# Performance work log

Hardware: AMD Instinct MI355X
Metric: run time of the kernel (lower is better)

The kernel has to match this reference:

```python
import jax, jax.numpy as jnp
import numpy as np

N_KW = 65536
N_DOC = 65536
N = N_KW + N_DOC
D_NODE = 128   # kw_size == middle_dim
D_MID = 128
D_FB = 16
D_T = 8
E = 1048576


def setup_inputs() -> dict:
    key = jax.random.key(0)
    ks = jax.random.split(key, 14)
    X_nodes = jax.random.normal(ks[0], (N, D_NODE), jnp.float32)
    X_feedback = jax.random.normal(ks[1], (N_DOC, D_FB), jnp.float32)
    X_time = jax.random.normal(ks[2], (N_DOC, D_T), jnp.float32)
    src = jax.random.randint(ks[3], (E,), 0, N_KW)            # kw node ids
    dst = N_KW + jax.random.randint(ks[4], (E,), 0, N_DOC)    # doc node ids
    edge_kw2doc = jnp.stack([src, dst])                       # [2, E], row0=src
    edge_doc2kw = jnp.stack([dst, src])

    def lin(k, fan_in, fan_out):
        return jax.random.normal(k, (fan_in, fan_out), jnp.float32) / np.sqrt(fan_in).astype(np.float32)

    params = dict(
        W0=lin(ks[5], D_NODE, D_MID), b0=jnp.zeros((D_MID,), jnp.float32),
        Wg1=lin(ks[6], D_MID, D_MID), bg1=jnp.zeros((D_MID,), jnp.float32),
        Wg2=lin(ks[7], D_MID, D_MID), bg2=jnp.zeros((D_MID,), jnp.float32),
        Wf1=lin(ks[8], D_FB, D_MID), bf1=jnp.zeros((D_MID,), jnp.float32),
        Wf2=lin(ks[9], D_MID, D_MID), bf2=jnp.zeros((D_MID,), jnp.float32),
        Wt1=lin(ks[10], D_T, D_MID), bt1=jnp.zeros((D_MID,), jnp.float32),
        Wt2=lin(ks[11], D_MID, D_MID), bt2=jnp.zeros((D_MID,), jnp.float32),
    )
    return {"X_nodes": X_nodes, "X_feedback": X_feedback, "X_time": X_time,
            "edge_kw2doc": edge_kw2doc, "edge_doc2kw": edge_doc2kw, "n_kw": N_KW, **params}


def _gcn(x, edge, W, b, n):
    # PyG GCNConv: add self-loops, symmetric normalization deg^{-1/2} A deg^{-1/2}, then linear.
    loop = jnp.arange(n)
    srcs = jnp.concatenate([edge[0], loop])
    dsts = jnp.concatenate([edge[1], loop])
    deg = jax.ops.segment_sum(jnp.ones(srcs.shape[0], x.dtype), dsts, num_segments=n)
    dis = jnp.where(deg > 0, jax.lax.rsqrt(jnp.maximum(deg, 1e-12)), jnp.zeros((), x.dtype))
    norm = dis[srcs] * dis[dsts]
    h = x @ W                                   # [N, D_MID]
    msg = h[srcs] * norm[:, None]               # gather on src, [E+N, D_MID]
    return jax.ops.segment_sum(msg, dsts, num_segments=n) + b


def reference(X_nodes, X_feedback, X_time, edge_kw2doc, edge_doc2kw, n_kw,
              W0, b0, Wg1, bg1, Wg2, bg2, Wf1, bf1, Wf2, bf2, Wt1, bt1, Wt2, bt2):
    n = X_nodes.shape[0]
    # feedback / time MLPs (relu on all but last layer)
    xf = jax.nn.relu(X_feedback @ Wf1 + bf1) @ Wf2 + bf2   # [N_DOC, D_MID]
    xt = jax.nn.relu(X_time @ Wt1 + bt1) @ Wt2 + bt2       # [N_DOC, D_MID]
    # layer 0: Linear on kw nodes only; doc rows stay zero
    x = jnp.zeros((n, W0.shape[1]), X_nodes.dtype)
    x = x.at[:n_kw].set(jax.nn.relu(X_nodes[:n_kw] @ W0 + b0))
    # layer 1: GCNConv kw2doc, write doc rows
    x2 = jax.nn.relu(_gcn(x, edge_kw2doc, Wg1, bg1, n))
    x = x.at[n_kw:].set(x2[n_kw:])
    # layer 2: GCNConv doc2kw, write kw rows
    x2 = jax.nn.relu(_gcn(x, edge_doc2kw, Wg2, bg2, n))
    x = x.at[:n_kw].set(x2[:n_kw])
    # merge_f (Mul) then merge_t (Mul) on doc rows
    x = x.at[n_kw:].mul(xf)
    x = x.at[n_kw:].mul(xt)
    return x
```

## Files before the change

### kernel.cpp

```cpp
#include <hip/hip_runtime.h>

#define NKW   65536
#define NDOC  65536
#define NSEG  131072
#define NE    1048576
#define CHUNK 4096
#define NBLK  (NE / CHUNK)

typedef unsigned long long u64;
typedef unsigned short     u16;
typedef unsigned int       u32;
typedef unsigned char      u8;

typedef __attribute__((ext_vector_type(8))) short short8;
typedef __attribute__((ext_vector_type(4))) float f32x4;
typedef __attribute__((ext_vector_type(2))) float f32x2;

union U8 { short8 v; u64 u[2]; short s[8]; };

__device__ __forceinline__ u16 f2bf(float f) {
    u32 u = __builtin_bit_cast(u32, f);
    u = (u + 0x7fffu + ((u >> 16) & 1u)) >> 16;
    return (u16)u;
}
__device__ __forceinline__ float bf2f(u16 h) {
    return __builtin_bit_cast(float, (u32)h << 16);
}
__device__ __forceinline__ u8 f2fp8(float f) {
    u32 pk = __builtin_amdgcn_cvt_pk_fp8_f32(f, f, 0u, false);
    return (u8)pk;
}

#define BUFA_OFF 0ull
#define BUFD_OFF 8388608ull
#define BUFB_OFF 16777216ull
#define BUFC_OFF 33554432ull
#define WF_OFF   50331648ull
#define CSR_OFF  51380224ull
#define CNT_OFF  59768832ull
#define AUX_OFF  60293120ull
#define OFF_OFF  60821504ull
#define DIS_OFF  61345792ull

#define WOFF_W0  0
#define WOFF_WG1 2048
#define WOFF_WG2 4096
#define WOFF_WF1 6144
#define WOFF_WF2 8192
#define WOFF_WT1 10240
#define WOFF_WT2 12288

struct PrepArgs { const float* w[7]; int K[7]; };

__global__ void zero_k(int* __restrict__ p) {
    p[blockIdx.x * 256 + threadIdx.x] = 0;
}

__global__ __launch_bounds__(256) void k1_hist_prep(
        const int* __restrict__ src, const int* __restrict__ dst,
        int* __restrict__ bhist, PrepArgs pa, short8* __restrict__ wfb) {
    __shared__ int h[512];
    const int tid = threadIdx.x;
    if (blockIdx.x < NBLK) {
        for (int i = tid; i < 512; i += 256) h[i] = 0;
        __syncthreads();
        int e0 = blockIdx.x * CHUNK;
        for (int i = tid; i < CHUNK; i += 256) {
            int s = src[e0 + i];
            int d = dst[e0 + i] - NKW;
            atomicAdd(&h[s >> 8], 1);
            atomicAdd(&h[256 + (d >> 8)], 1);
        }
        __syncthreads();
        for (int i = tid; i < 512; i += 256)
            if (h[i]) atomicAdd(&bhist[i], h[i]);
    } else {
        int u = (blockIdx.x - NBLK) * 4 + (tid >> 6);
        if (u < 224) {
            int m = u >> 5, bk = u & 31;
            int kc = bk >> 3, ct = bk & 7;
            int l = tid & 63;
            int K = pa.K[m];
            const float* W = pa.w[m];
            U8 o;
            #pragma unroll
            for (int i = 0; i < 8; ++i) {
                int k   = kc * 32 + 4 * (l >> 4) + (i & 3) + 16 * (i >> 2);
                int col = ct * 16 + (l & 15);
                float v = (k < K) ? W[(size_t)k * 128 + col] : 0.f;
                o.s[i] = (short)f2bf(v);
            }
            wfb[(size_t)m * 2048 + bk * 64 + l] = o.v;
        }
    }
}

__global__ __launch_bounds__(256) void k2_part(
        const int* __restrict__ src, const int* __restrict__ dst,
        const int* __restrict__ bhist, int* __restrict__ bfill,
        u32* __restrict__ pairs) {
    __shared__ int h[512], sc[512], base[512], gb[512];
    __shared__ u32 staged[2 * CHUNK];
    const int tid = threadIdx.x;

    for (int i = tid; i < 512; i += 256) gb[i] = bhist[i];
    __syncthreads();
    for (int d = 1; d < 512; d <<= 1) {
        int i1 = tid + 256;
        int t0 = (tid >= d) ? gb[tid - d] : 0;
        int t1 = gb[i1 - d];
        __syncthreads();
        gb[tid] += t0; gb[i1] += t1;
        __syncthreads();
    }
    for (int i = tid; i < 512; i += 256) gb[i] -= bhist[i];
    for (int i = tid; i < 512; i += 256) h[i] = 0;
    __syncthreads();

    const int e0 = blockIdx.x * CHUNK;
    int se[16], de[16];
    #pragma unroll
    for (int j = 0; j < 16; ++j) {
        int e = e0 + tid + j * 256;
        se[j] = src[e];
        de[j] = dst[e] - NKW;
        atomicAdd(&h[se[j] >> 8], 1);
        atomicAdd(&h[256 + (de[j] >> 8)], 1);
    }
    __syncthreads();

    sc[tid] = h[tid];
    __syncthreads();
    for (int d = 1; d < 256; d <<= 1) {
        int t = (tid >= d) ? sc[tid - d] : 0;
        __syncthreads();
        sc[tid] += t;
        __syncthreads();
    }
    sc[256 + tid] = h[256 + tid];
    __syncthreads();
    for (int d = 1; d < 256; d <<= 1) {
        int t = (tid >= d) ? sc[256 + tid - d] : 0;
        __syncthreads();
        sc[256 + tid] += t;
        __syncthreads();
    }

    for (int i = tid; i < 512; i += 256) {
        base[i] = gb[i] + atomicAdd(&bfill[i], h[i]);
        sc[i] -= h[i];
        h[i] = 0;
    }
    __syncthreads();

    #pragma unroll
    for (int j = 0; j < 16; ++j) {
        int bk = se[j] >> 8;
        int r  = atomicAdd(&h[bk], 1);
        staged[sc[bk] + r] = ((u32)(se[j] & 255) << 16) | (u32)de[j];
        int bd = 256 + (de[j] >> 8);
        int r2 = atomicAdd(&h[bd], 1);
        staged[CHUNK + sc[bd] + r2] = ((u32)(de[j] & 255) << 16) | (u32)se[j];
    }
    __syncthreads();

    for (int i = tid; i < 512; i += 256) {
        int n = h[i];
        int so = (i < 256 ? 0 : CHUNK) + sc[i];
        u32* dp = pairs + base[i];
        for (int j = 0; j < n; ++j) dp[j] = staged[so + j];
    }
}

__global__ __launch_bounds__(256) void k3_build(
        const u32* __restrict__ pairs, const int* __restrict__ bhist,
        int* __restrict__ off, int* __restrict__ cnt,
        float* __restrict__ dis, int* __restrict__ csr) {
    __shared__ int lcnt[256], loff[256], bs[256], gsc[512];
    const int tid = threadIdx.x;
    const int b = blockIdx.x;
    for (int i = tid; i < 512; i += 256) gsc[i] = bhist[i];
    __syncthreads();
    for (int d = 1; d < 512; d <<= 1) {
        int i1 = tid + 256;
        int t0 = (tid >= d) ? gsc[tid - d] : 0;
        int t1 = gsc[i1 - d];
        __syncthreads();
        gsc[tid] += t0; gsc[i1] += t1;
        __syncthreads();
    }
    const int size  = bhist[b];
    const int start = gsc[b] - size;
    lcnt[tid] = 0;
    __syncthreads();
    for (int i = tid; i < size; i += 256)
        atomicAdd(&lcnt[(pairs[start + i] >> 16) & 255], 1);
    __syncthreads();
    int s = lcnt[tid];
    bs[tid] = s;
    __syncthreads();
    for (int d = 1; d < 256; d <<= 1) {
        int t = (tid >= d) ? bs[tid - d] : 0;
        __syncthreads();
        bs[tid] += t;
        __syncthreads();
    }
    const int P = bs[tid] - s;
    const int seg = (b < 256) ? (b * 256 + tid) : (NKW + (b - 256) * 256 + tid);
    off[seg] = start + P;
    cnt[seg] = s;
    dis[seg] = rsqrtf((float)(s + 1));
    loff[tid] = P;
    lcnt[tid] = 0;
    __syncthreads();
    for (int i = tid; i < size; i += 256) {
        u32 p = pairs[start + i];
        int key = (p >> 16) & 255;
        int r = atomicAdd(&lcnt[key], 1);
        csr[start + loff[key] + r] = (int)(p & 0xFFFF);
    }
}

__global__ __launch_bounds__(256) void k45_gemm0_gates(
        const float* __restrict__ Xn, const short8* __restrict__ wfb,
        const float* __restrict__ b0, u8* __restrict__ h0f8,
        const float* __restrict__ Xfb, const float* __restrict__ Xt,
        const float* __restrict__ bf1v, const float* __restrict__ bf2v,
        const float* __restrict__ bt1v, const float* __restrict__ bt2v,
        u16* __restrict__ g) {
    __shared__ u16 H[64][136];
    const int tid = threadIdx.x;
    const int w = tid >> 6, l = tid & 63, lr = l & 15, q = l >> 4;

    if (blockIdx.x >= 1024) {
        const int blk = blockIdx.x - 1024;
        const int row = blk * 64 + w * 16 + lr;
        f32x4 acc[8];
        #pragma unroll
        for (int ct = 0; ct < 8; ++ct) acc[ct] = (f32x4){0.f, 0.f, 0.f, 0.f};
        #pragma unroll
        for (int kc = 0; kc < 4; ++kc) {
            U8 a;
            const int kb = kc * 32 + 4 * q;
            const float* A = Xn + (size_t)row * 128;
            f32x4 lo = *(const f32x4*)(A + kb);
            f32x4 hi = *(const f32x4*)(A + kb + 16);
            #pragma unroll
            for (int i = 0; i < 4; ++i) {
                a.s[i]     = (short)f2bf(lo[i]);
                a.s[4 + i] = (short)f2bf(hi[i]);
            }
            #pragma unroll
            for (int ct = 0; ct < 8; ++ct)
                acc[ct] = __builtin_amdgcn_mfma_f32_16x16x32_bf16(
                              a.v, wfb[WOFF_W0 + (kc * 8 + ct) * 64 + l], acc[ct], 0, 0, 0);
        }
        const int orow0 = blk * 64 + w * 16 + 4 * q;
        #pragma unroll
        for (int ct = 0; ct < 8; ++ct) {
            const int col = ct * 16 + lr;
            const float bb = b0[col];
            #pragma unroll
            for (int r = 0; r < 4; ++r) {
                float v = fmaxf(acc[ct][r] + bb, 0.f);
                h0f8[(size_t)(orow0 + r) * 128 + col] = f2fp8(v);
            }
        }
        return;
    }

    const int blk  = blockIdx.x;
    const int row0 = blk * 64 + w * 16;
    const int lrow = w * 16 + lr;
    const int orow = w * 16 + 4 * q;

    f32x4 acc[8];
    {
        U8 a;
        f32x4 x = *(const f32x4*)(Xfb + (size_t)(row0 + lr) * 16 + 4 * q);
        #pragma unroll
        for (int i = 0; i < 4; ++i) { a.s[i] = (short)f2bf(x[i]); a.s[4 + i] = 0; }
        #pragma unroll
        for (int ct = 0; ct < 8; ++ct)
            acc[ct] = __builtin_amdgcn_mfma_f32_16x16x32_bf16(
                          a.v, wfb[WOFF_WF1 + ct * 64 + l], (f32x4){0.f,0.f,0.f,0.f}, 0, 0, 0);
    }
    #pragma unroll
    for (int ct = 0; ct < 8; ++ct) {
        const int col = ct * 16 + lr;
        const float bb = bf1v[col];
        #pragma unroll
        for (int r = 0; r < 4; ++r)
            H[orow + r][col] = f2bf(fmaxf(acc[ct][r] + bb, 0.f));
    }
    __threadfence_block();

    f32x4 accf[8];
    #pragma unroll
    for (int ct = 0; ct < 8; ++ct) accf[ct] = (f32x4){0.f, 0.f, 0.f, 0.f};
    #pragma unroll
    for (int kc = 0; kc < 4; ++kc) {
        U8 a;
        const int kb = kc * 32 + 4 * q;
        a.u[0] = *(const u64*)&H[lrow][kb];
        a.u[1] = *(const u64*)&H[lrow][kb + 16];
        #pragma unroll
        for (int ct = 0; ct < 8; ++ct)
            accf[ct] = __builtin_amdgcn_mfma_f32_16x16x32_bf16(
                           a.v, wfb[WOFF_WF2 + (kc * 8 + ct) * 64 + l], accf[ct], 0, 0, 0);
    }
    __threadfence_block();

    {
        U8 a;
        #pragma unroll
        for (int i = 0; i < 8; ++i) a.s[i] = 0;
        if (q < 2) {
            f32x4 x = *(const f32x4*)(Xt + (size_t)(row0 + lr) * 8 + 4 * q);
            #pragma unroll
            for (int i = 0; i < 4; ++i) a.s[i] = (short)f2bf(x[i]);
        }
        #pragma unroll
        for (int ct = 0; ct < 8; ++ct)
            acc[ct] = __builtin_amdgcn_mfma_f32_16x16x32_bf16(
                          a.v, wfb[WOFF_WT1 + ct * 64 + l], (f32x4){0.f,0.f,0.f,0.f}, 0, 0, 0);
    }
    #pragma unroll
    for (int ct = 0; ct < 8; ++ct) {
        const int col = ct * 16 + lr;
        const float bb = bt1v[col];
        #pragma unroll
        for (int r = 0; r < 4; ++r)
            H[orow + r][col] = f2bf(fmaxf(acc[ct][r] + bb, 0.f));
    }
    __threadfence_block();

    f32x4 acct[8];
    #pragma unroll
    for (int ct = 0; ct < 8; ++ct) acct[ct] = (f32x4){0.f, 0.f, 0.f, 0.f};
    #pragma unroll
    for (int kc = 0; kc < 4; ++kc) {
        U8 a;
        const int kb = kc * 32 + 4 * q;
        a.u[0] = *(const u64*)&H[lrow][kb];
        a.u[1] = *(const u64*)&H[lrow][kb + 16];
        #pragma unroll
        for (int ct = 0; ct < 8; ++ct)
            acct[ct] = __builtin_amdgcn_mfma_f32_16x16x32_bf16(
                           a.v, wfb[WOFF_WT2 + (kc * 8 + ct) * 64 + l], acct[ct], 0, 0, 0);
    }
    #pragma unroll
    for (int ct = 0; ct < 8; ++ct) {
        const int col = ct * 16 + lr;
        const float b2f = bf2v[col];
        const float b2t = bt2v[col];
        #pragma unroll
        for (int r = 0; r < 4; ++r) {
            float gv = (accf[ct][r] + b2f) * (acct[ct][r] + b2t);
            g[(size_t)(blk * 64 + orow + r) * 128 + col] = f2bf(gv);
        }
    }
}

template<bool KW_SIDE>
__global__ __launch_bounds__(256) void aggf8_k(
        const int* __restrict__ off, const int* __restrict__ cnt,
        const int* __restrict__ csr, const u8* __restrict__ gsrc,
        const u8* __restrict__ h0f8, const float* __restrict__ dis,
        u16* __restrict__ outb) {
    const int r    = blockIdx.x * 16 + (threadIdx.x >> 4);
    const int lane = threadIdx.x & 15;
    const int seg  = KW_SIDE ? r : (NKW + r);
    const int st = off[seg];
    const int n  = cnt[seg];
    float a[8];
    #pragma unroll
    for (int j = 0; j < 8; ++j) a[j] = 0.f;

    #define DECACC(vv) { \
        u32 lo_ = (u32)(vv), hi_ = (u32)((vv) >> 32); \
        f32x2 p0 = __builtin_amdgcn_cvt_pk_f32_fp8(lo_, false); \
        f32x2 p1 = __builtin_amdgcn_cvt_pk_f32_fp8(lo_, true);  \
        f32x2 p2 = __builtin_amdgcn_cvt_pk_f32_fp8(hi_, false); \
        f32x2 p3 = __builtin_amdgcn_cvt_pk_f32_fp8(hi_, true);  \
        a[0] += p0[0]; a[1] += p0[1]; a[2] += p1[0]; a[3] += p1[1]; \
        a[4] += p2[0]; a[5] += p2[1]; a[6] += p3[0]; a[7] += p3[1]; }

    int i = 0;
    for (; i + 8 <= n; i += 8) {
        int nb[8];
        #pragma unroll
        for (int k = 0; k < 8; ++k) nb[k] = csr[st + i + k];
        u64 v[8];
        #pragma unroll
        for (int k = 0; k < 8; ++k)
            v[k] = *(const u64*)(gsrc + (size_t)nb[k] * 128 + lane * 8);
        #pragma unroll
        for (int k = 0; k < 8; ++k) DECACC(v[k])
    }
    for (; i < n; ++i) {
        int nb = csr[st + i];
        u64 v = *(const u64*)(gsrc + (size_t)nb * 128 + lane * 8);
        DECACC(v)
    }
    #undef DECACC

    const float dk = dis[seg];
    if (KW_SIDE) {
        u64 hv = *(const u64*)(h0f8 + (size_t)r * 128 + lane * 8);
        u32 lo_ = (u32)hv, hi_ = (u32)(hv >> 32);
        f32x2 p0 = __builtin_amdgcn_cvt_pk_f32_fp8(lo_, false);
        f32x2 p1 = __builtin_amdgcn_cvt_pk_f32_fp8(lo_, true);
        f32x2 p2 = __builtin_amdgcn_cvt_pk_f32_fp8(hi_, false);
        f32x2 p3 = __builtin_amdgcn_cvt_pk_f32_fp8(hi_, true);
        float hh[8] = {p0[0], p0[1], p1[0], p1[1], p2[0], p2[1], p3[0], p3[1]};
        #pragma unroll
        for (int j = 0; j < 8; ++j) a[j] = dk * (a[j] + dk * hh[j]);
    } else {
        #pragma unroll
        for (int j = 0; j < 8; ++j) a[j] *= dk;
    }
    U8 o;
    #pragma unroll
    for (int j = 0; j < 8; ++j) o.s[j] = (short)f2bf(a[j]);
    *(short8*)(outb + (size_t)r * 128 + lane * 8) = o.v;
}

__global__ __launch_bounds__(256) void k7_gemm1g(
        const u16* __restrict__ aggin, const short8* __restrict__ wfb,
        const float* __restrict__ bg1, const u16* __restrict__ gmul,
        u8* __restrict__ xdocf8, float* __restrict__ outdoc) {
    const int tid = threadIdx.x;
    const int w = tid >> 6, l = tid & 63, lr = l & 15, q = l >> 4;
    const int row = blockIdx.x * 64 + w * 16 + lr;
    f32x4 acc[8];
    #pragma unroll
    for (int ct = 0; ct < 8; ++ct) acc[ct] = (f32x4){0.f, 0.f, 0.f, 0.f};
    #pragma unroll
    for (int kc = 0; kc < 4; ++kc) {
        U8 a;
        const int kb = kc * 32 + 4 * q;
        const u16* A = aggin + (size_t)row * 128;
        a.u[0] = *(const u64*)(A + kb);
        a.u[1] = *(const u64*)(A + kb + 16);
        #pragma unroll
        for (int ct = 0; ct < 8; ++ct)
            acc[ct] = __builtin_amdgcn_mfma_f32_16x16x32_bf16(
                          a.v, wfb[WOFF_WG1 + (kc * 8 + ct) * 64 + l], acc[ct], 0, 0, 0);
    }
    const int orow0 = blockIdx.x * 64 + w * 16 + 4 * q;
    #pragma unroll
    for (int ct = 0; ct < 8; ++ct) {
        const int col = ct * 16 + lr;
        const float bb = bg1[col];
        #pragma unroll
        for (int r = 0; r < 4; ++r) {
            float v = fmaxf(acc[ct][r] + bb, 0.f);
            const size_t idx = (size_t)(orow0 + r) * 128 + col;
            xdocf8[idx] = f2fp8(v);
            float o = v * bf2f(gmul[idx]);
            __builtin_nontemporal_store(o, outdoc + idx);
        }
    }
}

__global__ __launch_bounds__(256) void k8_gemm2(
        const u16* __restrict__ Av, const short8* __restrict__ wfb,
        const float* __restrict__ bg2, float* __restrict__ outf32) {
    const int tid = threadIdx.x;
    const int w = tid >> 6, l = tid & 63, lr = l & 15, q = l >> 4;
    const int row = blockIdx.x * 64 + w * 16 + lr;
    f32x4 acc[8];
    #pragma unroll
    for (int ct = 0; ct < 8; ++ct) acc[ct] = (f32x4){0.f, 0.f, 0.f, 0.f};
    #pragma unroll
    for (int kc = 0; kc < 4; ++kc) {
        U8 a;
        const int kb = kc * 32 + 4 * q;
        const u16* A = Av + (size_t)row * 128;
        a.u[0] = *(const u64*)(A + kb);
        a.u[1] = *(const u64*)(A + kb + 16);
        #pragma unroll
        for (int ct = 0; ct < 8; ++ct)
            acc[ct] = __builtin_amdgcn_mfma_f32_16x16x32_bf16(
                          a.v, wfb[WOFF_WG2 + (kc * 8 + ct) * 64 + l], acc[ct], 0, 0, 0);
    }
    const int orow0 = blockIdx.x * 64 + w * 16 + 4 * q;
    #pragma unroll
    for (int ct = 0; ct < 8; ++ct) {
        const int col = ct * 16 + lr;
        const float bb = bg2[col];
        #pragma unroll
        for (int r = 0; r < 4; ++r) {
            float v = fmaxf(acc[ct][r] + bb, 0.f);
            __builtin_nontemporal_store(v, outf32 + (size_t)(orow0 + r) * 128 + col);
        }
    }
}

extern "C" void kernel_launch(void* const* d_in, const int* in_sizes, int n_in,
                              void* d_out, int out_size, void* d_ws, size_t ws_size,
                              hipStream_t stream) {
    const float* Xn  = (const float*)d_in[0];
    const float* Xfb = (const float*)d_in[1];
    const float* Xt  = (const float*)d_in[2];
    const int*   e01 = (const int*)d_in[3];
    const float* W0  = (const float*)d_in[6];
    const float* b0  = (const float*)d_in[7];
    const float* Wg1 = (const float*)d_in[8];
    const float* bg1 = (const float*)d_in[9];
    const float* Wg2 = (const float*)d_in[10];
    const float* bg2 = (const float*)d_in[11];
    const float* Wf1 = (const float*)d_in[12];
    const float* bf1 = (const float*)d_in[13];
    const float* Wf2 = (const float*)d_in[14];
    const float* bf2 = (const float*)d_in[15];
    const float* Wt1 = (const float*)d_in[16];
    const float* bt1 = (const float*)d_in[17];
    const float* Wt2 = (const float*)d_in[18];
    const float* bt2 = (const float*)d_in[19];

    float* out = (float*)d_out;
    char*  ws  = (char*)d_ws;
    u8*    bufA  = (u8*)(ws + BUFA_OFF);
    u8*    bufD  = (u8*)(ws + BUFD_OFF);
    u16*   bufB  = (u16*)(ws + BUFB_OFF);
    u16*   bufC  = (u16*)(ws + BUFC_OFF);
    u32*   pairs = (u32*)(ws + BUFC_OFF);
    short8* wfb  = (short8*)(ws + WF_OFF);
    int*   csr   = (int*)(ws + CSR_OFF);
    int*   cnt   = (int*)(ws + CNT_OFF);
    int*   bhist = (int*)(ws + AUX_OFF);
    int*   bfill = bhist + 512;
    int*   off   = (int*)(ws + OFF_OFF);
    float* dis   = (float*)(ws + DIS_OFF);

    const int* src = e01;
    const int* dst = e01 + NE;

    PrepArgs pa;
    pa.w[0] = W0;  pa.K[0] = 128;
    pa.w[1] = Wg1; pa.K[1] = 128;
    pa.w[2] = Wg2; pa.K[2] = 128;
    pa.w[3] = Wf1; pa.K[3] = 16;
    pa.w[4] = Wf2; pa.K[4] = 128;
    pa.w[5] = Wt1; pa.K[5] = 8;
    pa.w[6] = Wt2; pa.K[6] = 128;

    zero_k<<<4, 256, 0, stream>>>(bhist);
    k1_hist_prep<<<NBLK + 56, 256, 0, stream>>>(src, dst, bhist, pa, wfb);
    k2_part<<<NBLK, 256, 0, stream>>>(src, dst, bhist, bfill, pairs);
    k3_build<<<512, 256, 0, stream>>>(pairs, bhist, off, cnt, dis, csr);
    k45_gemm0_gates<<<2048, 256, 0, stream>>>(Xn, wfb, b0, bufA,
                                              Xfb, Xt, bf1, bf2, bt1, bt2, bufB);

    aggf8_k<false><<<NDOC / 16, 256, 0, stream>>>(off, cnt, csr, bufA, nullptr, dis, bufC);
    k7_gemm1g<<<1024, 256, 0, stream>>>(bufC, wfb, bg1, bufB, bufD,
                                        out + (size_t)NKW * 128);

    aggf8_k<true><<<NKW / 16, 256, 0, stream>>>(off, cnt, csr, bufD, bufA, dis, bufC);
    k8_gemm2<<<1024, 256, 0, stream>>>(bufC, wfb, bg2, out);
}
```

Before: 166.1 us.

## Fuse gate MLP into partition kernel and gemm0 into CSR build kernel

Merges the independent feedback/time gate MLP blocks into the edge-partition launch and the layer-0 GEMM blocks into the CSR build launch, removing one kernel launch. Independent work now runs alongside the latency-bound graph preprocessing kernels and can fill idle CUs. The gate blocks reuse the partition kernel's shared staging buffer for their H tile. The partition kernel's larger shared footprint now applies to the gate blocks too, which may lower their occupancy.

```diff
diff --git a/kernel.cpp b/kernel.cpp
--- a/kernel.cpp
+++ b/kernel.cpp
@@ -95,181 +95,93 @@
     }
 }
 
-__global__ __launch_bounds__(256) void k2_part(
+__global__ __launch_bounds__(256) void k2_part_gates(
         const int* __restrict__ src, const int* __restrict__ dst,
         const int* __restrict__ bhist, int* __restrict__ bfill,
-        u32* __restrict__ pairs) {
-    __shared__ int h[512], sc[512], base[512], gb[512];
-    __shared__ u32 staged[2 * CHUNK];
-    const int tid = threadIdx.x;
-
-    for (int i = tid; i < 512; i += 256) gb[i] = bhist[i];
-    __syncthreads();
-    for (int d = 1; d < 512; d <<= 1) {
-        int i1 = tid + 256;
-        int t0 = (tid >= d) ? gb[tid - d] : 0;
-        int t1 = gb[i1 - d];
-        __syncthreads();
-        gb[tid] += t0; gb[i1] += t1;
-        __syncthreads();
-    }
-    for (int i = tid; i < 512; i += 256) gb[i] -= bhist[i];
-    for (int i = tid; i < 512; i += 256) h[i] = 0;
-    __syncthreads();
-
-    const int e0 = blockIdx.x * CHUNK;
-    int se[16], de[16];
-    #pragma unroll
-    for (int j = 0; j < 16; ++j) {
-        int e = e0 + tid + j * 256;
-        se[j] = src[e];
-        de[j] = dst[e] - NKW;
-        atomicAdd(&h[se[j] >> 8], 1);
-        atomicAdd(&h[256 + (de[j] >> 8)], 1);
-    }
-    __syncthreads();
-
-    sc[tid] = h[tid];
-    __syncthreads();
-    for (int d = 1; d < 256; d <<= 1) {
-        int t = (tid >= d) ? sc[tid - d] : 0;
-        __syncthreads();
-        sc[tid] += t;
-        __syncthreads();
-    }
-    sc[256 + tid] = h[256 + tid];
-    __syncthreads();
-    for (int d = 1; d < 256; d <<= 1) {
-        int t = (tid >= d) ? sc[256 + tid - d] : 0;
-        __syncthreads();
-        sc[256 + tid] += t;
-        __syncthreads();
-    }
-
-    for (int i = tid; i < 512; i += 256) {
-        base[i] = gb[i] + atomicAdd(&bfill[i], h[i]);
-        sc[i] -= h[i];
-        h[i] = 0;
-    }
-    __syncthreads();
-
-    #pragma unroll
-    for (int j = 0; j < 16; ++j) {
-        int bk = se[j] >> 8;
-        int r  = atomicAdd(&h[bk], 1);
-        staged[sc[bk] + r] = ((u32)(se[j] & 255) << 16) | (u32)de[j];
-        int bd = 256 + (de[j] >> 8);
-        int r2 = atomicAdd(&h[bd], 1);
-        staged[CHUNK + sc[bd] + r2] = ((u32)(de[j] & 255) << 16) | (u32)se[j];
-    }
-    __syncthreads();
-
-    for (int i = tid; i < 512; i += 256) {
-        int n = h[i];
-        int so = (i < 256 ? 0 : CHUNK) + sc[i];
-        u32* dp = pairs + base[i];
-        for (int j = 0; j < n; ++j) dp[j] = staged[so + j];
-    }
-}
-
-__global__ __launch_bounds__(256) void k3_build(
-        const u32* __restrict__ pairs, const int* __restrict__ bhist,
-        int* __restrict__ off, int* __restrict__ cnt,
-        float* __restrict__ dis, int* __restrict__ csr) {
-    __shared__ int lcnt[256], loff[256], bs[256], gsc[512];
-    const int tid = threadIdx.x;
-    const int b = blockIdx.x;
-    for (int i = tid; i < 512; i += 256) gsc[i] = bhist[i];
-    __syncthreads();
-    for (int d = 1; d < 512; d <<= 1) {
-        int i1 = tid + 256;
-        int t0 = (tid >= d) ? gsc[tid - d] : 0;
-        int t1 = gsc[i1 - d];
-        __syncthreads();
-        gsc[tid] += t0; gsc[i1] += t1;
-        __syncthreads();
-    }
-    const int size  = bhist[b];
-    const int start = gsc[b] - size;
-    lcnt[tid] = 0;
-    __syncthreads();
-    for (int i = tid; i < size; i += 256)
-        atomicAdd(&lcnt[(pairs[start + i] >> 16) & 255], 1);
-    __syncthreads();
-    int s = lcnt[tid];
-    bs[tid] = s;
-    __syncthreads();
-    for (int d = 1; d < 256; d <<= 1) {
-        int t = (tid >= d) ? bs[tid - d] : 0;
-        __syncthreads();
-        bs[tid] += t;
-        __syncthreads();
-    }
-    const int P = bs[tid] - s;
-    const int seg = (b < 256) ? (b * 256 + tid) : (NKW + (b - 256) * 256 + tid);
-    off[seg] = start + P;
-    cnt[seg] = s;
-    dis[seg] = rsqrtf((float)(s + 1));
-    loff[tid] = P;
-    lcnt[tid] = 0;
-    __syncthreads();
-    for (int i = tid; i < size; i += 256) {
-        u32 p = pairs[start + i];
-        int key = (p >> 16) & 255;
-        int r = atomicAdd(&lcnt[key], 1);
-        csr[start + loff[key] + r] = (int)(p & 0xFFFF);
-    }
-}
-
-__global__ __launch_bounds__(256) void k45_gemm0_gates(
-        const float* __restrict__ Xn, const short8* __restrict__ wfb,
-        const float* __restrict__ b0, u8* __restrict__ h0f8,
+        u32* __restrict__ pairs,
+        const short8* __restrict__ wfb,
         const float* __restrict__ Xfb, const float* __restrict__ Xt,
         const float* __restrict__ bf1v, const float* __restrict__ bf2v,
         const float* __restrict__ bt1v, const float* __restrict__ bt2v,
         u16* __restrict__ g) {
-    __shared__ u16 H[64][136];
+    __shared__ int h[512], sc[512], base[512], gb[512];
+    __shared__ u32 staged[2 * CHUNK];
     const int tid = threadIdx.x;
+
+    if (blockIdx.x < NBLK) {
+        for (int i = tid; i < 512; i += 256) gb[i] = bhist[i];
+        __syncthreads();
+        for (int d = 1; d < 512; d <<= 1) {
+            int i1 = tid + 256;
+            int t0 = (tid >= d) ? gb[tid - d] : 0;
+            int t1 = gb[i1 - d];
+            __syncthreads();
+            gb[tid] += t0; gb[i1] += t1;
+            __syncthreads();
+        }
+        for (int i = tid; i < 512; i += 256) gb[i] -= bhist[i];
+        for (int i = tid; i < 512; i += 256) h[i] = 0;
+        __syncthreads();
+
+        const int e0 = blockIdx.x * CHUNK;
+        int se[16], de[16];
+        #pragma unroll
+        for (int j = 0; j < 16; ++j) {
+            int e = e0 + tid + j * 256;
+            se[j] = src[e];
+            de[j] = dst[e] - NKW;
+            atomicAdd(&h[se[j] >> 8], 1);
+            atomicAdd(&h[256 + (de[j] >> 8)], 1);
+        }
+        __syncthreads();
+
+        sc[tid] = h[tid];
+        __syncthreads();
+        for (int d = 1; d < 256; d <<= 1) {
+            int t = (tid >= d) ? sc[tid - d] : 0;
+            __syncthreads();
+            sc[tid] += t;
+            __syncthreads();
+        }
+        sc[256 + tid] = h[256 + tid];
+        __syncthreads();
+        for (int d = 1; d < 256; d <<= 1) {
+            int t = (tid >= d) ? sc[256 + tid - d] : 0;
+            __syncthreads();
+            sc[256 + tid] += t;
+            __syncthreads();
+        }
+
+        for (int i = tid; i < 512; i += 256) {
+            base[i] = gb[i] + atomicAdd(&bfill[i], h[i]);
+            sc[i] -= h[i];
+            h[i] = 0;
+        }
+        __syncthreads();
+
+        #pragma unroll
+        for (int j = 0; j < 16; ++j) {
+            int bk = se[j] >> 8;
+            int r  = atomicAdd(&h[bk], 1);
+            staged[sc[bk] + r] = ((u32)(se[j] & 255) << 16) | (u32)de[j];
+            int bd = 256 + (de[j] >> 8);
+            int r2 = atomicAdd(&h[bd], 1);
+            staged[CHUNK + sc[bd] + r2] = ((u32)(de[j] & 255) << 16) | (u32)se[j];
+        }
+        __syncthreads();
+
+        for (int i = tid; i < 512; i += 256) {
+            int n = h[i];
+            int so = (i < 256 ? 0 : CHUNK) + sc[i];
+            u32* dp = pairs + base[i];
+            for (int j = 0; j < n; ++j) dp[j] = staged[so + j];
+        }
+        return;
+    }
+
+    u16 (*H)[136] = (u16(*)[136])staged;
     const int w = tid >> 6, l = tid & 63, lr = l & 15, q = l >> 4;
-
-    if (blockIdx.x >= 1024) {
-        const int blk = blockIdx.x - 1024;
-        const int row = blk * 64 + w * 16 + lr;
-        f32x4 acc[8];
-        #pragma unroll
-        for (int ct = 0; ct < 8; ++ct) acc[ct] = (f32x4){0.f, 0.f, 0.f, 0.f};
-        #pragma unroll
-        for (int kc = 0; kc < 4; ++kc) {
-            U8 a;
-            const int kb = kc * 32 + 4 * q;
-            const float* A = Xn + (size_t)row * 128;
-            f32x4 lo = *(const f32x4*)(A + kb);
-            f32x4 hi = *(const f32x4*)(A + kb + 16);
-            #pragma unroll
-            for (int i = 0; i < 4; ++i) {
-                a.s[i]     = (short)f2bf(lo[i]);
-                a.s[4 + i] = (short)f2bf(hi[i]);
-            }
-            #pragma unroll
-            for (int ct = 0; ct < 8; ++ct)
-                acc[ct] = __builtin_amdgcn_mfma_f32_16x16x32_bf16(
-                              a.v, wfb[WOFF_W0 + (kc * 8 + ct) * 64 + l], acc[ct], 0, 0, 0);
-        }
-        const int orow0 = blk * 64 + w * 16 + 4 * q;
-        #pragma unroll
-        for (int ct = 0; ct < 8; ++ct) {
-            const int col = ct * 16 + lr;
-            const float bb = b0[col];
-            #pragma unroll
-            for (int r = 0; r < 4; ++r) {
-                float v = fmaxf(acc[ct][r] + bb, 0.f);
-                h0f8[(size_t)(orow0 + r) * 128 + col] = f2fp8(v);
-            }
-        }
-        return;
-    }
-
-    const int blk  = blockIdx.x;
+    const int blk  = blockIdx.x - NBLK;
     const int row0 = blk * 64 + w * 16;
     const int lrow = w * 16 + lr;
     const int orow = w * 16 + 4 * q;
@@ -358,6 +270,96 @@
         for (int r = 0; r < 4; ++r) {
             float gv = (accf[ct][r] + b2f) * (acct[ct][r] + b2t);
             g[(size_t)(blk * 64 + orow + r) * 128 + col] = f2bf(gv);
+        }
+    }
+}
+
+__global__ __launch_bounds__(256) void k3_build_gemm0(
+        const u32* __restrict__ pairs, const int* __restrict__ bhist,
+        int* __restrict__ off, int* __restrict__ cnt,
+        float* __restrict__ dis, int* __restrict__ csr,
+        const float* __restrict__ Xn, const short8* __restrict__ wfb,
+        const float* __restrict__ b0, u8* __restrict__ h0f8) {
+    __shared__ int lcnt[256], loff[256], bs[256], gsc[512];
+    const int tid = threadIdx.x;
+
+    if (blockIdx.x < 512) {
+        const int b = blockIdx.x;
+        for (int i = tid; i < 512; i += 256) gsc[i] = bhist[i];
+        __syncthreads();
+        for (int d = 1; d < 512; d <<= 1) {
+            int i1 = tid + 256;
+            int t0 = (tid >= d) ? gsc[tid - d] : 0;
+            int t1 = gsc[i1 - d];
+            __syncthreads();
+            gsc[tid] += t0; gsc[i1] += t1;
+            __syncthreads();
+        }
+        const int size  = bhist[b];
+        const int start = gsc[b] - size;
+        lcnt[tid] = 0;
+        __syncthreads();
+        for (int i = tid; i < size; i += 256)
+            atomicAdd(&lcnt[(pairs[start + i] >> 16) & 255], 1);
+        __syncthreads();
+        int s = lcnt[tid];
+        bs[tid] = s;
+        __syncthreads();
+        for (int d = 1; d < 256; d <<= 1) {
+            int t = (tid >= d) ? bs[tid - d] : 0;
+            __syncthreads();
+            bs[tid] += t;
+            __syncthreads();
+        }
+        const int P = bs[tid] - s;
+        const int seg = (b < 256) ? (b * 256 + tid) : (NKW + (b - 256) * 256 + tid);
+        off[seg] = start + P;
+        cnt[seg] = s;
+        dis[seg] = rsqrtf((float)(s + 1));
+        loff[tid] = P;
+        lcnt[tid] = 0;
+        __syncthreads();
+        for (int i = tid; i < size; i += 256) {
+            u32 p = pairs[start + i];
+            int key = (p >> 16) & 255;
+            int r = atomicAdd(&lcnt[key], 1);
+            csr[start + loff[key] + r] = (int)(p & 0xFFFF);
+        }
+        return;
+    }
+
+    const int blk = blockIdx.x - 512;
+    const int w = tid >> 6, l = tid & 63, lr = l & 15, q = l >> 4;
+    const int row = blk * 64 + w * 16 + lr;
+    f32x4 acc[8];
+    #pragma unroll
+    for (int ct = 0; ct < 8; ++ct) acc[ct] = (f32x4){0.f, 0.f, 0.f, 0.f};
+    #pragma unroll
+    for (int kc = 0; kc < 4; ++kc) {
+        U8 a;
+        const int kb = kc * 32 + 4 * q;
+        const float* A = Xn + (size_t)row * 128;
+        f32x4 lo = *(const f32x4*)(A + kb);
+        f32x4 hi = *(const f32x4*)(A + kb + 16);
+        #pragma unroll
+        for (int i = 0; i < 4; ++i) {
+            a.s[i]     = (short)f2bf(lo[i]);
+            a.s[4 + i] = (short)f2bf(hi[i]);
+        }
+        #pragma unroll
+        for (int ct = 0; ct < 8; ++ct)
+            acc[ct] = __builtin_amdgcn_mfma_f32_16x16x32_bf16(
+                          a.v, wfb[WOFF_W0 + (kc * 8 + ct) * 64 + l], acc[ct], 0, 0, 0);
+    }
+    const int orow0 = blk * 64 + w * 16 + 4 * q;
+    #pragma unroll
+    for (int ct = 0; ct < 8; ++ct) {
+        const int col = ct * 16 + lr;
+        const float bb = b0[col];
+        #pragma unroll
+        for (int r = 0; r < 4; ++r) {
+            float v = fmaxf(acc[ct][r] + bb, 0.f);
+            h0f8[(size_t)(orow0 + r) * 128 + col] = f2fp8(v);
         }
     }
 }
@@ -549,10 +551,11 @@
 
     zero_k<<<4, 256, 0, stream>>>(bhist);
     k1_hist_prep<<<NBLK + 56, 256, 0, stream>>>(src, dst, bhist, pa, wfb);
-    k2_part<<<NBLK, 256, 0, stream>>>(src, dst, bhist, bfill, pairs);
-    k3_build<<<512, 256, 0, stream>>>(pairs, bhist, off, cnt, dis, csr);
-    k45_gemm0_gates<<<2048, 256, 0, stream>>>(Xn, wfb, b0, bufA,
-                                              Xfb, Xt, bf1, bf2, bt1, bt2, bufB);
+    k2_part_gates<<<NBLK + 1024, 256, 0, stream>>>(
+        src, dst, bhist, bfill, pairs,
+        wfb, Xfb, Xt, bf1, bf2, bt1, bt2, bufB);
+    k3_build_gemm0<<<512 + 1024, 256, 0, stream>>>(
+        pairs, bhist, off, cnt, dis, csr, Xn, wfb, b0, bufA);
 
     aggf8_k<false><<<NDOC / 16, 256, 0, stream>>>(off, cnt, csr, bufA, nullptr, dis, bufC);
     k7_gemm1g<<<1024, 256, 0, stream>>>(bufC, wfb, bg1, bufB, bufD,
```

New measurement: 155.8 us (median of 2 runs). -6.2%, faster.
